# Optimization experiments

Measured on AMD Instinct MI355X. Metric: run time of the kernel, lower is better.

Reference implementation:

```python
import jax, jax.numpy as jnp
import numpy as np

DIM = 512
HEADS = 8
DHEAD = DIM // HEADS
M = DIM // 2          # num_landmarks = 256
ITERS = 6             # pinv iterations
KSIZE = 33            # residual conv kernel (seq axis)
EPS = 1e-5            # LayerNorm eps (torch default)


def moore_penrose_pinv(a, iters=ITERS):
    # a: [b, h, m, m]; iterative Newton-Schulz style pseudo-inverse
    abs_a = jnp.abs(a)
    col = abs_a.sum(-1).max()   # global max of row-sums
    row = abs_a.sum(-2).max()   # global max of col-sums
    z = jnp.swapaxes(a, -1, -2) / (col * row)
    I = jnp.eye(a.shape[-1], dtype=a.dtype)

    def body(z, _):
        az = a @ z
        z = 0.25 * z @ (13.0 * I - az @ (15.0 * I - az @ (7.0 * I - az)))
        return z, None

    z, _ = jax.lax.scan(body, z, None, length=iters)
    return z


def res_conv(v, conv_w):
    # v: [b, h, n, d] treated as NCHW (C=heads), depthwise kernel (33, 1)
    return jax.lax.conv_general_dilated(
        v, conv_w, window_strides=(1, 1),
        padding=((KSIZE // 2, KSIZE // 2), (0, 0)),
        dimension_numbers=('NCHW', 'OIHW', 'NCHW'),
        feature_group_count=HEADS)


def setup_inputs() -> dict:
    key = jax.random.key(0)
    ks = jax.random.split(key, 5)
    b, n = 4, 4096  # n % M == 0 -> no padding branch
    x = jax.random.normal(ks[0], (b, n, DIM), jnp.float32)
    norm_w = jnp.ones((DIM,), jnp.float32)
    norm_b = jnp.zeros((DIM,), jnp.float32)
    Wqkv = jax.random.normal(ks[1], (DIM, 3 * DIM), jnp.float32) * (DIM ** -0.5)
    Wout = jax.random.normal(ks[2], (DIM, DIM), jnp.float32) * (DIM ** -0.5)
    bout = jnp.zeros((DIM,), jnp.float32)
    conv_w = jax.random.normal(ks[3], (HEADS, 1, KSIZE, 1), jnp.float32) * 0.05
    return {"x": x, "norm_w": norm_w, "norm_b": norm_b,
            "Wqkv": Wqkv, "Wout": Wout, "bout": bout, "conv_w": conv_w}


def reference(x, norm_w, norm_b, Wqkv, Wout, bout, conv_w):
    b, n, dim = x.shape
    # LayerNorm
    mu = x.mean(-1, keepdims=True)
    var = ((x - mu) ** 2).mean(-1, keepdims=True)
    xn = (x - mu) * jax.lax.rsqrt(var + EPS) * norm_w + norm_b

    # QKV projection, split heads: [b, h, n, d]
    qkv = xn @ Wqkv
    q, k, v = jnp.split(qkv, 3, axis=-1)
    sh = lambda t: t.reshape(b, n, HEADS, DHEAD).transpose(0, 2, 1, 3)
    q, k, v = sh(q), sh(k), sh(v)
    q = q * (DHEAD ** -0.5)

    # landmarks: mean over consecutive segments of length l = n // M
    l = n // M
    q_l = q.reshape(b, HEADS, M, l, DHEAD).mean(3)  # [b,h,m,d]
    k_l = k.reshape(b, HEADS, M, l, DHEAD).mean(3)

    sim1 = jnp.einsum('bhid,bhjd->bhij', q, k_l)    # [b,h,n,m]
    sim2 = jnp.einsum('bhid,bhjd->bhij', q_l, k_l)  # [b,h,m,m]
    sim3 = jnp.einsum('bhid,bhjd->bhij', q_l, k)    # [b,h,m,n]
    a1 = jax.nn.softmax(sim1, axis=-1)
    a2 = jax.nn.softmax(sim2, axis=-1)
    a3 = jax.nn.softmax(sim3, axis=-1)

    a2_inv = moore_penrose_pinv(a2)
    out = (a1 @ a2_inv) @ (a3 @ v)                  # [b,h,n,d]
    out = out + res_conv(v, conv_w)                  # residual depthwise conv on v

    out = out.transpose(0, 2, 1, 3).reshape(b, n, dim)
    out = out @ Wout + bout                          # to_out (dropout = identity in eval)
    return x + out                                   # TransLayer residual
```

## Files before the change

### kernel.cpp

```cpp
#include <hip/hip_runtime.h>
#include <hip/hip_bf16.h>

#define BB 4
#define NN 4096
#define DIMM 512
#define HH 8
#define DD 64
#define MM 256
#define LL 16
#define BHH 32
#define NROW (BB*NN)
#define KS 33

typedef __attribute__((ext_vector_type(8))) short short8;
typedef __attribute__((ext_vector_type(4))) float float4v;

static __device__ __forceinline__ unsigned short bf16_bits(float v) {
    __hip_bfloat16 h = __float2bfloat16(v);
    return *reinterpret_cast<unsigned short*>(&h);
}

static __device__ __forceinline__ void gl_lds16(const void* g, void* l) {
    __builtin_amdgcn_global_load_lds((const __attribute__((address_space(1))) void*)g,
                                     (__attribute__((address_space(3))) void*)l, 16, 0, 0);
}

static __device__ __forceinline__ void bar_nv() {
    asm volatile("s_waitcnt lgkmcnt(0)\ns_barrier" ::: "memory");
}

static __device__ __forceinline__ int xcd_swz(int hw, int nwg) {
    return (hw & 7) * (nwg >> 3) + (hw >> 3);
}

__launch_bounds__(256)
__global__ void ln_kernel(const float* __restrict__ x,
                          const float* __restrict__ w,
                          const float* __restrict__ bvec,
                          __hip_bfloat16* __restrict__ xn) {
    int row = blockIdx.x;
    int t = threadIdx.x;
    const float* xr = x + (long)row * DIMM;
    float v0 = xr[t];
    float v1 = xr[t + 256];
    __shared__ float red[256];
    red[t] = v0 + v1;
    __syncthreads();
    for (int off = 128; off > 0; off >>= 1) { if (t < off) red[t] += red[t + off]; __syncthreads(); }
    float mu = red[0] * (1.0f / DIMM);
    __syncthreads();
    float d0 = v0 - mu, d1 = v1 - mu;
    red[t] = d0 * d0 + d1 * d1;
    __syncthreads();
    for (int off = 128; off > 0; off >>= 1) { if (t < off) red[t] += red[t + off]; __syncthreads(); }
    float var = red[0] * (1.0f / DIMM);
    float rs = rsqrtf(var + 1e-5f);
    xn[(long)row * DIMM + t]       = __float2bfloat16(d0 * rs * w[t]       + bvec[t]);
    xn[(long)row * DIMM + t + 256] = __float2bfloat16(d1 * rs * w[t + 256] + bvec[t + 256]);
}

__launch_bounds__(256)
__global__ void transpose_bf16(const float* __restrict__ in, __hip_bfloat16* __restrict__ outp,
                               int K, int N) {
    __shared__ float tile[32][33];
    int k0 = blockIdx.y * 32, n0 = blockIdx.x * 32;
    int tx = threadIdx.x & 31, ty = threadIdx.x >> 5;
    #pragma unroll
    for (int i = 0; i < 32; i += 8)
        tile[ty + i][tx] = in[(long)(k0 + ty + i) * N + n0 + tx];
    __syncthreads();
    #pragma unroll
    for (int i = 0; i < 32; i += 8)
        outp[(long)(n0 + ty + i) * K + k0 + tx] = __float2bfloat16(tile[tx][ty + i]);
}

enum { EPI_NONE = 0, EPI_QKV = 1, EPI_OUT = 2 };

template<int EPI>
__launch_bounds__(256)
__global__ void gemm_mfma(const __hip_bfloat16* __restrict__ A,
                          const __hip_bfloat16* __restrict__ Bt,
                          float* __restrict__ C, int M, int N, int K,
                          const float* __restrict__ bias,
                          const float* __restrict__ resid,
                          __hip_bfloat16* __restrict__ qb,
                          __hip_bfloat16* __restrict__ kb,
                          __hip_bfloat16* __restrict__ vtb) {
    __shared__ __hip_bfloat16 As[128][64];
    __shared__ __hip_bfloat16 Bs[128][64];
    const int t = threadIdx.x;
    const int hw = blockIdx.y * gridDim.x + blockIdx.x;
    const int lg = xcd_swz(hw, gridDim.x * gridDim.y);
    const int m0 = (lg / gridDim.x) * 128, n0 = (lg % gridDim.x) * 128;
    const int wave = t >> 6, lane = t & 63;
    const int wrow = wave >> 1, wcol = wave & 1;
    const int lm = lane & 15, quad = lane >> 4;
    const int wbase = wave * 64;

    const __hip_bfloat16* gA[4];
    const __hip_bfloat16* gB[4];
    __hip_bfloat16* lA[4];
    __hip_bfloat16* lB[4];
    #pragma unroll
    for (int p = 0; p < 4; ++p) {
        int idx = t + p * 256;
        int r = idx >> 3;
        int csrc = ((idx & 7) ^ (r & 7)) * 8;
        int cb = (p * 256 + wbase) * 8;
        gA[p] = &A[(long)(m0 + r) * K + csrc];
        gB[p] = &Bt[(long)(n0 + r) * K + csrc];
        lA[p] = &As[0][0] + cb;
        lB[p] = &Bs[0][0] + cb;
    }

    const __hip_bfloat16* pA[2][4];
    const __hip_bfloat16* pB[2][4];
    #pragma unroll
    for (int i = 0; i < 4; ++i) {
        int ra = wrow * 64 + i * 16 + lm;
        int rb = wcol * 64 + i * 16 + lm;
        int ca = quad ^ (ra & 3), ra2 = (ra >> 2) & 1;
        int cb2 = quad ^ (rb & 3), rb2 = (rb >> 2) & 1;
        pA[0][i] = &As[ra][(4 * ra2       + ca)  * 8];
        pA[1][i] = &As[ra][(4 * (1 - ra2) + ca)  * 8];
        pB[0][i] = &Bs[rb][(4 * rb2       + cb2) * 8];
        pB[1][i] = &Bs[rb][(4 * (1 - rb2) + cb2) * 8];
    }

    float4v acc[4][4] = {};

    for (int k0 = 0; k0 < K; k0 += 64) {
        #pragma unroll
        for (int p = 0; p < 4; ++p) {
            gl_lds16(gA[p], lA[p]);
            gl_lds16(gB[p], lB[p]);
            gA[p] += 64;
            gB[p] += 64;
        }
        __syncthreads();
        #pragma unroll
        for (int ksu = 0; ksu < 2; ++ksu) {
            short8 af[4], bfr[4];
            #pragma unroll
            for (int i = 0; i < 4; ++i) {
                af[i]  = *(const short8*)pA[ksu][i];
                bfr[i] = *(const short8*)pB[ksu][i];
            }
            #pragma unroll
            for (int i = 0; i < 4; ++i)
                #pragma unroll
                for (int j = 0; j < 4; ++j)
                    acc[i][j] = __builtin_amdgcn_mfma_f32_16x16x32_bf16(af[i], bfr[j], acc[i][j], 0, 0, 0);
        }
        __syncthreads();
    }

    #pragma unroll
    for (int i = 0; i < 4; ++i) {
        #pragma unroll
        for (int j = 0; j < 4; ++j) {
            int rowb = m0 + wrow * 64 + i * 16 + quad * 4;
            int col  = n0 + wcol * 64 + j * 16 + lm;
            if (EPI == EPI_QKV) {
                int b = rowb >> 12, seq = rowb & (NN - 1);
                int which = col >> 9, rem = col & 511;
                int h = rem >> 6, dd = rem & 63;
                int bh = b * HH + h;
                if (which == 0) {
                    #pragma unroll
                    for (int r = 0; r < 4; ++r)
                        qb[((long)bh * NN + seq + r) * DD + dd] = __float2bfloat16(acc[i][j][r] * 0.125f);
                } else if (which == 1) {
                    #pragma unroll
                    for (int r = 0; r < 4; ++r)
                        kb[((long)bh * NN + seq + r) * DD + dd] = __float2bfloat16(acc[i][j][r]);
                } else {
                    union { unsigned long long u; unsigned short s[4]; } pk;
                    #pragma unroll
                    for (int r = 0; r < 4; ++r) pk.s[r] = bf16_bits(acc[i][j][r]);
                    *(unsigned long long*)&vtb[((long)bh * DD + dd) * NN + seq] = pk.u;
                }
            } else {
                #pragma unroll
                for (int r = 0; r < 4; ++r) {
                    int row = rowb + r;
                    C[(long)row * N + col] = acc[i][j][r] + bias[col] + resid[(long)row * N + col];
                }
            }
        }
    }
}

__launch_bounds__(256)
__global__ void gemm_pinv(const __hip_bfloat16* __restrict__ A,
                          const __hip_bfloat16* __restrict__ Bt,
                          __hip_bfloat16* __restrict__ CnBf,
                          float* __restrict__ CnF,
                          __hip_bfloat16* __restrict__ CTbf,
                          float diag, float sgn, float scale) {
    __shared__ __hip_bfloat16 As[64][256];
    __shared__ __hip_bfloat16 Bs[64][256];
    const int t = threadIdx.x;
    const int hw = (blockIdx.z * 4 + blockIdx.y) * 4 + blockIdx.x;
    const int lg = xcd_swz(hw, 512);
    const long base = (long)(lg >> 4) << 16;
    const int m0 = ((lg >> 2) & 3) * 64, n0 = (lg & 3) * 64;
    const int wave = t >> 6, lane = t & 63;
    const int wr = wave >> 1, wc = wave & 1;
    const int lm = lane & 15, quad = lane >> 4;
    const __hip_bfloat16* Ab = A + base;
    const __hip_bfloat16* Bb = Bt + base;

    #pragma unroll
    for (int p = 0; p < 8; ++p) {
        int idx = t + p * 256;
        int r = idx >> 5;
        int csrc = ((idx & 31) ^ (r & 7)) * 8;
        int cb = idx * 8;
        gl_lds16(&Ab[(long)(m0 + r) * 256 + csrc], &As[0][0] + cb);
        gl_lds16(&Bb[(long)(n0 + r) * 256 + csrc], &Bs[0][0] + cb);
    }

    const char* pA[2][2];
    const char* pB[2][2];
    #pragma unroll
    for (int i = 0; i < 2; ++i) {
        int ra = wr * 32 + i * 16 + lm;
        int rb = wc * 32 + i * 16 + lm;
        int ca = quad ^ (ra & 3), ra2 = (ra >> 2) & 1;
        int cb2 = quad ^ (rb & 3), rb2 = (rb >> 2) & 1;
        pA[0][i] = (const char*)&As[ra][(4 * ra2       + ca)  * 8];
        pA[1][i] = (const char*)&As[ra][(4 * (1 - ra2) + ca)  * 8];
        pB[0][i] = (const char*)&Bs[rb][(4 * rb2       + cb2) * 8];
        pB[1][i] = (const char*)&Bs[rb][(4 * (1 - rb2) + cb2) * 8];
    }
    __syncthreads();

    float4v acc[2][2] = {};
    #pragma unroll
    for (int ksu = 0; ksu < 8; ++ksu) {
        short8 af[2], bfr[2];
        #pragma unroll
        for (int i = 0; i < 2; ++i) {
            af[i]  = *(const short8*)(pA[ksu & 1][i] + (ksu >> 1) * 128);
            bfr[i] = *(const short8*)(pB[ksu & 1][i] + (ksu >> 1) * 128);
        }
        #pragma unroll
        for (int i = 0; i < 2; ++i)
            #pragma unroll
            for (int j = 0; j < 2; ++j)
                acc[i][j] = __builtin_amdgcn_mfma_f32_16x16x32_bf16(af[i], bfr[j], acc[i][j], 0, 0, 0);
    }

    #pragma unroll
    for (int i = 0; i < 2; ++i)
        #pragma unroll
        for (int j = 0; j < 2; ++j) {
            const int rowb = wr * 32 + i * 16 + quad * 4;
            const int col  = wc * 32 + j * 16 + lm;
            union { unsigned long long u; unsigned short s[4]; } pk;
            #pragma unroll
            for (int r = 0; r < 4; ++r) {
                float v = acc[i][j][r] * scale;
                long off = base + (long)(m0 + rowb + r) * 256 + n0 + col;
                if (CnBf) CnBf[off] = __float2bfloat16(v);
                if (CnF)  CnF[off]  = v;
                float tv = sgn * v + ((m0 + rowb + r) == (n0 + col) ? diag : 0.0f);
                pk.s[r] = bf16_bits(tv);
            }
            if (CTbf)
                *(unsigned long long*)&CTbf[base + (long)(n0 + col) * 256 + m0 + rowb] = pk.u;
        }
}

__launch_bounds__(256)
__global__ void pinv_prep(const float* __restrict__ a2, const float* __restrict__ scl,
                          __hip_bfloat16* __restrict__ a2bf, __hip_bfloat16* __restrict__ z0T,
                          __hip_bfloat16* __restrict__ z0n) {
    __shared__ float tl[64][65];
    const int t = threadIdx.x;
    const long base = (long)blockIdx.z << 16;
    const int i0 = blockIdx.y * 64, j0 = blockIdx.x * 64;
    float s = scl[0];
    #pragma unroll
    for (int p = 0; p < 16; ++p) {
        int idx = t + p * 256;
        int r = idx >> 6, c = idx & 63;
        long off = base + (long)(i0 + r) * 256 + j0 + c;
        float v = a2[off];
        a2bf[off] = __float2bfloat16(v);
        float zv = v * s;
        z0T[off] = __float2bfloat16(zv);
        tl[r][c] = zv;
    }
    __syncthreads();
    int r = t & 63;
    #pragma unroll
    for (int u = 0; u < 16; ++u) {
        int c = u * 4 + (t >> 6);
        z0n[base + (long)(j0 + c) * 256 + i0 + r] = __float2bfloat16(tl[r][c]);
    }
}

template<int EPI, bool TRANSB>
__launch_bounds__(256)
__global__ void gemm64(const float* __restrict__ A, const float* __restrict__ Bm,
                       float* __restrict__ C,
                       int M, int N, int K, long sA, long sB, long sC, float alpha) {
    const int gx = gridDim.x, gxy = gridDim.x * gridDim.y;
    const int hw = blockIdx.z * gxy + blockIdx.y * gx + blockIdx.x;
    const int lg = xcd_swz(hw, gxy * gridDim.z);
    const int bz = lg / gxy;
    const int rem = lg % gxy;
    const float* Ab = A + (long)bz * sA;
    const float* Bb = Bm + (long)bz * sB;
    float* Cb = C + (long)bz * sC;

    __shared__ float As[16][64];
    __shared__ float Bs[16][64];

    const int tid = threadIdx.x;
    const int tx = tid & 15;
    const int ty = tid >> 4;
    const int m0 = (rem / gx) * 64;
    const int n0 = (rem % gx) * 64;

    float acc[4][4] = {};

    for (int k0 = 0; k0 < K; k0 += 16) {
        {
            int r  = tid >> 2;
            int kk = (tid & 3) * 4;
            float4 va = *(const float4*)(Ab + (long)(m0 + r) * K + k0 + kk);
            As[kk + 0][r] = va.x; As[kk + 1][r] = va.y; As[kk + 2][r] = va.z; As[kk + 3][r] = va.w;
        }
        if (!TRANSB) {
            int kk = tid >> 4;
            int j  = (tid & 15) * 4;
            float4 vb = *(const float4*)(Bb + (long)(k0 + kk) * N + n0 + j);
            Bs[kk][j + 0] = vb.x; Bs[kk][j + 1] = vb.y; Bs[kk][j + 2] = vb.z; Bs[kk][j + 3] = vb.w;
        } else {
            int j  = tid >> 2;
            int kk = (tid & 3) * 4;
            float4 vb = *(const float4*)(Bb + (long)(n0 + j) * K + k0 + kk);
            Bs[kk + 0][j] = vb.x; Bs[kk + 1][j] = vb.y; Bs[kk + 2][j] = vb.z; Bs[kk + 3][j] = vb.w;
        }
        __syncthreads();
        #pragma unroll
        for (int kk = 0; kk < 16; ++kk) {
            float a0 = As[kk][ty * 4 + 0], a1 = As[kk][ty * 4 + 1];
            float a2 = As[kk][ty * 4 + 2], a3 = As[kk][ty * 4 + 3];
            float b0 = Bs[kk][tx * 4 + 0], b1 = Bs[kk][tx * 4 + 1];
            float b2 = Bs[kk][tx * 4 + 2], b3 = Bs[kk][tx * 4 + 3];
            acc[0][0] += a0 * b0; acc[0][1] += a0 * b1; acc[0][2] += a0 * b2; acc[0][3] += a0 * b3;
            acc[1][0] += a1 * b0; acc[1][1] += a1 * b1; acc[1][2] += a1 * b2; acc[1][3] += a1 * b3;
            acc[2][0] += a2 * b0; acc[2][1] += a2 * b1; acc[2][2] += a2 * b2; acc[2][3] += a2 * b3;
            acc[3][0] += a3 * b0; acc[3][1] += a3 * b1; acc[3][2] += a3 * b2; acc[3][3] += a3 * b3;
        }
        __syncthreads();
    }

    #pragma unroll
    for (int r = 0; r < 4; ++r)
        #pragma unroll
        for (int c = 0; c < 4; ++c)
            Cb[(long)(m0 + ty * 4 + r) * N + n0 + tx * 4 + c] = acc[r][c] * alpha;
}

__global__ void landmark_kernel(const __hip_bfloat16* __restrict__ qb,
                                const __hip_bfloat16* __restrict__ kb,
                                float* __restrict__ q_l, float* __restrict__ k_l,
                                __hip_bfloat16* __restrict__ q_lb,
                                __hip_bfloat16* __restrict__ k_lb) {
    int bh = blockIdx.x >> 8;
    int m  = blockIdx.x & 255;
    int d  = threadIdx.x;
    const __hip_bfloat16* src = (blockIdx.y ? kb : qb) + ((long)bh * NN + m * LL) * DD + d;
    float s = 0.f;
    #pragma unroll
    for (int t = 0; t < LL; ++t) s += __bfloat162float(src[(long)t * DD]);
    s *= (1.0f / LL);
    long off = ((long)bh * MM + m) * DD + d;
    if (blockIdx.y) { k_l[off] = s; k_lb[off] = __float2bfloat16(s); }
    else            { q_l[off] = s; q_lb[off] = __float2bfloat16(s); }
}

__launch_bounds__(256)
__global__ void softmax256_kernel(float* __restrict__ a) {
    long row = blockIdx.x;
    int t = threadIdx.x;
    float* r = a + row * 256;
    float v = r[t];
    __shared__ float red[256];
    red[t] = v;
    __syncthreads();
    for (int off = 128; off > 0; off >>= 1) { if (t < off) red[t] = fmaxf(red[t], red[t + off]); __syncthreads(); }
    float mx = red[0];
    __syncthreads();
    float e = __expf(v - mx);
    red[t] = e;
    __syncthreads();
    for (int off = 128; off > 0; off >>= 1) { if (t < off) red[t] += red[t + off]; __syncthreads(); }
    r[t] = e / red[0];
}

__launch_bounds__(256)
__global__ void redmax_kernel(const float* __restrict__ a2, float* __restrict__ red) {
    int blk = blockIdx.x;
    int bh = blk >> 3, cg = blk & 7;
    int t = threadIdx.x;
    const float* Ab = a2 + ((long)bh << 16) + cg * 32;
    int c = t & 31, rg = t >> 5;
    float s = 0.f;
    for (int r = rg * 32; r < rg * 32 + 32; ++r) s += Ab[(long)r * 256 + c];
    __shared__ float m[256];
    m[t] = s;
    __syncthreads();
    if (t < 32) {
        float cs = 0.f;
        #pragma unroll
        for (int g = 0; g < 8; ++g) cs += m[t + 32 * g];
        m[t] = cs;
    }
    __syncthreads();
    if (t == 0) {
        float mx = m[0];
        #pragma unroll
        for (int i = 1; i < 32; ++i) mx = fmaxf(mx, m[i]);
        red[blk] = mx;
    }
}

__launch_bounds__(256)
__global__ void scale_kernel(const float* __restrict__ red, float* __restrict__ scl) {
    __shared__ float b[256];
    int t = threadIdx.x;
    b[t] = red[t];
    __syncthreads();
    for (int off = 128; off > 0; off >>= 1) {
        if (t < off) b[t] = fmaxf(b[t], b[t + off]);
        __syncthreads();
    }
    if (t == 0) scl[0] = 1.0f / b[0];
}

__launch_bounds__(256)
__global__ void a3v_mfma(const __hip_bfloat16* __restrict__ qlb,
                         const __hip_bfloat16* __restrict__ kb,
                         const __hip_bfloat16* __restrict__ vtb,
                         float* __restrict__ opart, float* __restrict__ lpart) {
    const int hw = blockIdx.y * 16 + blockIdx.x;
    const int lg = xcd_swz(hw, 512);
    const int bh = lg >> 4;
    const int mt = (lg >> 2) & 3;
    const int ns = lg & 3;
    const int t = threadIdx.x;
    const int wave = t >> 6, lane = t & 63;
    const int wr = wave >> 1, wc = wave & 1;
    const int lm = lane & 15, quad = lane >> 4;
    const int r8 = t >> 3, c8 = (t & 7) * 8;

    __shared__ __hip_bfloat16 Qs[64][72];
    __shared__ __hip_bfloat16 Ks[64][72];
    __shared__ __hip_bfloat16 Vt[64][72];
    __shared__ __hip_bfloat16 Ps[64][72];
    __shared__ float lredS[64][2];

    {
        const __hip_bfloat16* qbase = qlb + ((long)bh * MM + mt * 64) * DD;
        *(uint4*)&Qs[r8][c8]      = *(const uint4*)&qbase[(long)r8 * DD + c8];
        *(uint4*)&Qs[r8 + 32][c8] = *(const uint4*)&qbase[(long)(r8 + 32) * DD + c8];
    }

    float4v acc[2][2] = {};
    float lacc[2][4] = {};
    const __hip_bfloat16* kbase = kb + ((long)bh * NN + ns * 1024) * DD;
    const __hip_bfloat16* vbase = vtb + (long)bh * DD * NN + ns * 1024;

    uint4 kv0 = *(const uint4*)&kbase[(long)r8 * DD + c8];
    uint4 kv1 = *(const uint4*)&kbase[(long)(r8 + 32) * DD + c8];
    uint4 vv0 = *(const uint4*)&vbase[(long)r8 * NN + c8];
    uint4 vv1 = *(const uint4*)&vbase[(long)(r8 + 32) * NN + c8];
    bar_nv();

    for (int ch = 0; ch < 16; ++ch) {
        *(uint4*)&Ks[r8][c8]      = kv0;
        *(uint4*)&Ks[r8 + 32][c8] = kv1;
        *(uint4*)&Vt[r8][c8]      = vv0;
        *(uint4*)&Vt[r8 + 32][c8] = vv1;
        if (ch < 15) {
            kv0 = *(const uint4*)&kbase[(long)((ch + 1) * 64 + r8) * DD + c8];
            kv1 = *(const uint4*)&kbase[(long)((ch + 1) * 64 + r8 + 32) * DD + c8];
            vv0 = *(const uint4*)&vbase[(long)r8 * NN + (ch + 1) * 64 + c8];
            vv1 = *(const uint4*)&vbase[(long)(r8 + 32) * NN + (ch + 1) * 64 + c8];
        }
        bar_nv();

        float4v s[2][2] = {};
        #pragma unroll
        for (int ks = 0; ks < 64; ks += 32) {
            short8 af[2], bfr[2];
            #pragma unroll
            for (int i = 0; i < 2; ++i) {
                af[i]  = *(const short8*)&Qs[wr * 32 + i * 16 + lm][ks + quad * 8];
                bfr[i] = *(const short8*)&Ks[wc * 32 + i * 16 + lm][ks + quad * 8];
            }
            #pragma unroll
            for (int i = 0; i < 2; ++i)
                #pragma unroll
                for (int j = 0; j < 2; ++j)
                    s[i][j] = __builtin_amdgcn_mfma_f32_16x16x32_bf16(af[i], bfr[j], s[i][j], 0, 0, 0);
        }
        #pragma unroll
        for (int i = 0; i < 2; ++i)
            #pragma unroll
            for (int j = 0; j < 2; ++j)
                #pragma unroll
                for (int r2 = 0; r2 < 4; ++r2) {
                    float e = __expf(s[i][j][r2]);
                    lacc[i][r2] += e;
                    Ps[wr * 32 + i * 16 + quad * 4 + r2][wc * 32 + j * 16 + lm] = __float2bfloat16(e);
                }
        bar_nv();

        #pragma unroll
        for (int ks = 0; ks < 64; ks += 32) {
            short8 af[2], bfr[2];
            #pragma unroll
            for (int i = 0; i < 2; ++i) {
                af[i]  = *(const short8*)&Ps[wr * 32 + i * 16 + lm][ks + quad * 8];
                bfr[i] = *(const short8*)&Vt[wc * 32 + i * 16 + lm][ks + quad * 8];
            }
            #pragma unroll
            for (int i = 0; i < 2; ++i)
                #pragma unroll
                for (int j = 0; j < 2; ++j)
                    acc[i][j] = __builtin_amdgcn_mfma_f32_16x16x32_bf16(af[i], bfr[j], acc[i][j], 0, 0, 0);
        }
        bar_nv();
    }

    #pragma unroll
    for (int i = 0; i < 2; ++i)
        #pragma unroll
        for (int r2 = 0; r2 < 4; ++r2) {
            float s = lacc[i][r2];
            s += __shfl_xor(s, 1);
            s += __shfl_xor(s, 2);
            s += __shfl_xor(s, 4);
            s += __shfl_xor(s, 8);
            if (lm == 0) lredS[wr * 32 + i * 16 + quad * 4 + r2][wc] = s;
        }
    __syncthreads();
    if (t < 64)
        lpart[((bh * 4 + mt) * 4 + ns) * 64 + t] = lredS[t][0] + lredS[t][1];
    const long pbase = ((long)((bh * 4 + mt) * 4 + ns)) << 12;
    #pragma unroll
    for (int i = 0; i < 2; ++i)
        #pragma unroll
        for (int j = 0; j < 2; ++j)
            #pragma unroll
            for (int r2 = 0; r2 < 4; ++r2)
                opart[pbase + (long)(wr * 32 + i * 16 + quad * 4 + r2) * 64 + wc * 32 + j * 16 + lm] = acc[i][j][r2];
}

__global__ void a3v_combine(const float* __restrict__ opart, const float* __restrict__ lpart,
                            float* __restrict__ a3v) {
    int idx = blockIdx.x * 256 + threadIdx.x;
    int d  = idx & 63;
    int m  = (idx >> 6) & 255;
    int bh = idx >> 14;
    int mt = m >> 6, r = m & 63;
    int pb = (bh * 4 + mt) * 4;
    float osum = 0.f, lsum = 0.f;
    #pragma unroll
    for (int ns = 0; ns < 4; ++ns) {
        osum += opart[(((long)(pb + ns)) << 12) + r * 64 + d];
        lsum += lpart[(pb + ns) * 64 + r];
    }
    a3v[((long)bh * MM + m) * DD + d] = osum / lsum;
}

__launch_bounds__(256)
__global__ void wmT_kernel(const float* __restrict__ wm, __hip_bfloat16* __restrict__ wtb) {
    __shared__ float tile[64][65];
    const int bh = blockIdx.x;
    const int t = threadIdx.x;
    for (int mc = 0; mc < 4; ++mc) {
        #pragma unroll
        for (int p = 0; p < 16; ++p) {
            int idx = t + p * 256;
            int r = idx >> 6, c = idx & 63;
            tile[r][c] = wm[((long)bh * MM + mc * 64 + r) * DD + c];
        }
        __syncthreads();
        #pragma unroll
        for (int p = 0; p < 16; ++p) {
            int idx = t + p * 256;
            int dd = idx >> 6, m = idx & 63;
            wtb[((long)bh * DD + dd) * MM + mc * 64 + m] = __float2bfloat16(tile[m][dd]);
        }
        __syncthreads();
    }
}

__launch_bounds__(256)
__global__ void attn_out_mfma(const __hip_bfloat16* __restrict__ qb,
                              const __hip_bfloat16* __restrict__ klb,
                              const __hip_bfloat16* __restrict__ wtb,
                              const __hip_bfloat16* __restrict__ vtb,
                              const float* __restrict__ convw,
                              __hip_bfloat16* __restrict__ ctx) {
    const int hw = blockIdx.y * 64 + blockIdx.x;
    const int lg = xcd_swz(hw, 2048);
    const int bh = lg >> 6;
    const int b = bh >> 3, h = bh & 7;
    const int i0 = (lg & 63) * 64;
    const int t = threadIdx.x;
    const int wave = t >> 6, lane = t & 63;
    const int wr = wave >> 1, wc = wave & 1;
    const int lm = lane & 15, quad = lane >> 4;
    const int r8 = t >> 3, c8 = (t & 7) * 8;

    __shared__ __hip_bfloat16 Qs[64][72];
    __shared__ __hip_bfloat16 KW[2][64][72];
    __shared__ __hip_bfloat16 Ps[64][72];
    __shared__ __hip_bfloat16 Vc[64][104];
    __shared__ float lredS[64][2];
    __shared__ float dsum[64];
    __shared__ float cwS[KS];
    __hip_bfloat16 (*Tpl)[104] = reinterpret_cast<__hip_bfloat16 (*)[104]>(&KW[0][0][0]);

    if (t < KS) cwS[t] = convw[h * KS + t];

    {
        const __hip_bfloat16* qbase = qb + ((long)bh * NN + i0) * DD;
        *(uint4*)&Qs[r8][c8]      = *(const uint4*)&qbase[(long)r8 * DD + c8];
        *(uint4*)&Qs[r8 + 32][c8] = *(const uint4*)&qbase[(long)(r8 + 32) * DD + c8];
    }
    {
        for (int c = t; c < 768; c += 256) {
            int dd = c / 12, u = c - dd * 12;
            int g0 = i0 - 16 + u * 8;
            const __hip_bfloat16* vrow = vtb + ((long)bh * DD + dd) * NN;
            __align__(16) __hip_bfloat16 tmp[8];
            if (g0 >= 0 && g0 + 8 <= NN) {
                *(uint4*)tmp = *(const uint4*)&vrow[g0];
            } else {
                #pragma unroll
                for (int e = 0; e < 8; ++e) {
                    int g = g0 + e;
                    tmp[e] = (g >= 0 && g < NN) ? vrow[g] : __float2bfloat16(0.f);
                }
            }
            *(uint4*)&Vc[dd][u * 8] = *(uint4*)tmp;
        }
    }
    __syncthreads();

    {
        int r  = t >> 2;
        int c0 = (t & 3) * 24;
        #pragma unroll
        for (int u = 0; u < 12; ++u) {
            int c = c0 + u * 2;
            int d0 = c - r, d1 = c + 1 - r;
            unsigned short lo = (d0 >= 0 && d0 < KS) ? bf16_bits(cwS[d0]) : (unsigned short)0;
            unsigned short hi = (d1 >= 0 && d1 < KS) ? bf16_bits(cwS[d1]) : (unsigned short)0;
            *(unsigned*)&Tpl[r][c] = ((unsigned)hi << 16) | lo;
        }
    }
    bar_nv();

    const __hip_bfloat16* klbase = klb + (long)bh * MM * DD;
    const __hip_bfloat16* wbase  = wtb + (long)bh * DD * MM;
    uint4 kv0 = *(const uint4*)&klbase[(long)r8 * DD + c8];
    uint4 kv1 = *(const uint4*)&klbase[(long)(r8 + 32) * DD + c8];
    uint4 wv0 = *(const uint4*)&wbase[(long)r8 * MM + c8];
    uint4 wv1 = *(const uint4*)&wbase[(long)(r8 + 32) * MM + c8];

    float4v accC[2][2] = {};
    #pragma unroll
    for (int ks = 0; ks < 96; ks += 32) {
        short8 af[2], bfr[2];
        #pragma unroll
        for (int i = 0; i < 2; ++i) {
            af[i]  = *(const short8*)&Tpl[wr * 32 + i * 16 + lm][ks + quad * 8];
            bfr[i] = *(const short8*)&Vc[wc * 32 + i * 16 + lm][ks + quad * 8];
        }
        #pragma unroll
        for (int i = 0; i < 2; ++i)
            #pragma unroll
            for (int j = 0; j < 2; ++j)
                accC[i][j] = __builtin_amdgcn_mfma_f32_16x16x32_bf16(af[i], bfr[j], accC[i][j], 0, 0, 0);
    }
    bar_nv();

    float4v acc[2][2] = {};
    float lacc[2][4] = {};

    for (int ch = 0; ch < 4; ++ch) {
        *(uint4*)&KW[0][r8][c8]      = kv0;
        *(uint4*)&KW[0][r8 + 32][c8] = kv1;
        *(uint4*)&KW[1][r8][c8]      = wv0;
        *(uint4*)&KW[1][r8 + 32][c8] = wv1;
        if (ch < 3) {
            kv0 = *(const uint4*)&klbase[(long)((ch + 1) * 64 + r8) * DD + c8];
            kv1 = *(const uint4*)&klbase[(long)((ch + 1) * 64 + r8 + 32) * DD + c8];
            wv0 = *(const uint4*)&wbase[(long)r8 * MM + (ch + 1) * 64 + c8];
            wv1 = *(const uint4*)&wbase[(long)(r8 + 32) * MM + (ch + 1) * 64 + c8];
        }
        bar_nv();

        float4v s[2][2] = {};
        #pragma unroll
        for (int ks = 0; ks < 64; ks += 32) {
            short8 af[2], bfr[2];
            #pragma unroll
            for (int i = 0; i < 2; ++i) {
                af[i]  = *(const short8*)&Qs[wr * 32 + i * 16 + lm][ks + quad * 8];
                bfr[i] = *(const short8*)&KW[0][wc * 32 + i * 16 + lm][ks + quad * 8];
            }
            #pragma unroll
            for (int i = 0; i < 2; ++i)
                #pragma unroll
                for (int j = 0; j < 2; ++j)
                    s[i][j] = __builtin_amdgcn_mfma_f32_16x16x32_bf16(af[i], bfr[j], s[i][j], 0, 0, 0);
        }
        #pragma unroll
        for (int i = 0; i < 2; ++i)
            #pragma unroll
            for (int j = 0; j < 2; ++j)
                #pragma unroll
                for (int r2 = 0; r2 < 4; ++r2) {
                    float e = __expf(s[i][j][r2]);
                    lacc[i][r2] += e;
                    Ps[wr * 32 + i * 16 + quad * 4 + r2][wc * 32 + j * 16 + lm] = __float2bfloat16(e);
                }
        bar_nv();

        #pragma unroll
        for (int ks = 0; ks < 64; ks += 32) {
            short8 af[2], bfr[2];
            #pragma unroll
            for (int i = 0; i < 2; ++i) {
                af[i]  = *(const short8*)&Ps[wr * 32 + i * 16 + lm][ks + quad * 8];
                bfr[i] = *(const short8*)&KW[1][wc * 32 + i * 16 + lm][ks + quad * 8];
            }
            #pragma unroll
            for (int i = 0; i < 2; ++i)
                #pragma unroll
                for (int j = 0; j < 2; ++j)
                    acc[i][j] = __builtin_amdgcn_mfma_f32_16x16x32_bf16(af[i], bfr[j], acc[i][j], 0, 0, 0);
        }
        bar_nv();
    }

    #pragma unroll
    for (int i = 0; i < 2; ++i)
        #pragma unroll
        for (int r2 = 0; r2 < 4; ++r2) {
            float s = lacc[i][r2];
            s += __shfl_xor(s, 1);
            s += __shfl_xor(s, 2);
            s += __shfl_xor(s, 4);
            s += __shfl_xor(s, 8);
            if (lm == 0) lredS[wr * 32 + i * 16 + quad * 4 + r2][wc] = s;
        }
    __syncthreads();
    if (t < 64) dsum[t] = 1.0f / (lredS[t][0] + lredS[t][1]);
    __syncthreads();

    #pragma unroll
    for (int j = 0; j < 2; ++j) {
        int dd = wc * 32 + j * 16 + lm;
        #pragma unroll
        for (int i = 0; i < 2; ++i) {
            int R = wr * 32 + i * 16 + quad * 4;
            #pragma unroll
            for (int r2 = 0; r2 < 4; ++r2) {
                int row = R + r2;
                ctx[((long)b * NN + i0 + row) * DIMM + h * DD + dd] =
                    __float2bfloat16(acc[i][j][r2] * dsum[row] + accC[i][j][r2]);
            }
        }
    }
}

extern "C" void kernel_launch(void* const* d_in, const int* in_sizes, int n_in,
                              void* d_out, int out_size, void* d_ws, size_t ws_size,
                              hipStream_t stream) {
    const float* x      = (const float*)d_in[0];
    const float* norm_w = (const float*)d_in[1];
    const float* norm_b = (const float*)d_in[2];
    const float* Wqkv   = (const float*)d_in[3];
    const float* Wout   = (const float*)d_in[4];
    const float* bout   = (const float*)d_in[5];
    const float* conv_w = (const float*)d_in[6];
    float* out = (float*)d_out;

    float* ws = (float*)d_ws;
    size_t o = 0;
    auto alloc = [&](size_t n) { float* p = ws + o; o += n; return p; };
    auto allocb = [&](size_t n) { return (__hip_bfloat16*)alloc((n + 1) / 2); };

    __hip_bfloat16* xn_bf  = allocb((size_t)NROW * DIMM);
    __hip_bfloat16* wqt_bf = allocb((size_t)3 * DIMM * DIMM);
    __hip_bfloat16* wot_bf = allocb((size_t)DIMM * DIMM);
    __hip_bfloat16* ctx_bf = allocb((size_t)NROW * DIMM);
    __hip_bfloat16* q_bf   = allocb((size_t)BHH * NN * DD);
    __hip_bfloat16* k_bf   = allocb((size_t)BHH * NN * DD);
    __hip_bfloat16* vt_bf  = allocb((size_t)BHH * DD * NN);
    __hip_bfloat16* qlb    = allocb((size_t)BHH * MM * DD);
    __hip_bfloat16* klb    = allocb((size_t)BHH * MM * DD);
    __hip_bfloat16* wt_bf  = allocb((size_t)BHH * DD * MM);
    float* q_l  = alloc((size_t)BHH * MM * DD);
    float* k_l  = alloc((size_t)BHH * MM * DD);
    float* a2   = alloc((size_t)BHH * MM * MM);
    float* zb   = alloc((size_t)BHH * MM * MM);
    float* az   = alloc((size_t)BHH * MM * MM);
    float* gb   = alloc((size_t)BHH * MM * MM);
    float* tb   = alloc((size_t)BHH * MM * MM);
    float* z2   = alloc((size_t)BHH * MM * MM);
    float* a3v  = alloc((size_t)BHH * MM * DD);
    float* wm   = alloc((size_t)BHH * MM * DD);
    float* opart = alloc((size_t)BHH * 4 * 4 * 64 * 64);
    float* lpart = alloc((size_t)BHH * 4 * 4 * 64);
    float* red  = alloc(256);
    float* scl  = alloc(64);

    const size_t HB = 1048576;
    __hip_bfloat16* a2bf = (__hip_bfloat16*)az;
    __hip_bfloat16* znA  = (__hip_bfloat16*)(az + HB);
    __hip_bfloat16* znB  = (__hip_bfloat16*)gb;
    __hip_bfloat16* zTA  = (__hip_bfloat16*)(gb + HB);
    __hip_bfloat16* zTB  = (__hip_bfloat16*)tb;
    __hip_bfloat16* azbf = (__hip_bfloat16*)(tb + HB);
    __hip_bfloat16* g1T  = (__hip_bfloat16*)z2;
    __hip_bfloat16* g2T  = (__hip_bfloat16*)(z2 + HB);
    __hip_bfloat16* g3T  = (__hip_bfloat16*)opart;

    ln_kernel<<<NROW, 256, 0, stream>>>(x, norm_w, norm_b, xn_bf);

    transpose_bf16<<<dim3(3 * DIMM / 32, DIMM / 32), 256, 0, stream>>>(Wqkv, wqt_bf, DIMM, 3 * DIMM);
    transpose_bf16<<<dim3(DIMM / 32, DIMM / 32), 256, 0, stream>>>(Wout, wot_bf, DIMM, DIMM);

    gemm_mfma<EPI_QKV><<<dim3(3 * DIMM / 128, NROW / 128), 256, 0, stream>>>(
        xn_bf, wqt_bf, nullptr, NROW, 3 * DIMM, DIMM,
        nullptr, nullptr, q_bf, k_bf, vt_bf);

    landmark_kernel<<<dim3(BHH * MM, 2), 64, 0, stream>>>(q_bf, k_bf, q_l, k_l, qlb, klb);

    gemm64<EPI_NONE, true><<<dim3(4, 4, BHH), 256, 0, stream>>>(
        q_l, k_l, a2, MM, MM, DD, (long)MM * DD, (long)MM * DD, (long)MM * MM, 1.0f);

    softmax256_kernel<<<BHH * MM, 256, 0, stream>>>(a2);

    redmax_kernel<<<BHH * 8, 256, 0, stream>>>(a2, red);
    scale_kernel<<<1, 256, 0, stream>>>(red, scl);

    dim3 g512(4, 4, BHH);
    pinv_prep<<<g512, 256, 0, stream>>>(a2, scl, a2bf, zTA, znA);

    __hip_bfloat16 *zn = znA, *zT = zTA, *zn2 = znB, *zT2 = zTB;
    for (int it = 0; it < 6; ++it) {
        gemm_pinv<<<g512, 256, 0, stream>>>(a2bf, zT, azbf, nullptr, g1T, 7.0f, -1.0f, 1.0f);
        gemm_pinv<<<g512, 256, 0, stream>>>(azbf, g1T, nullptr, nullptr, g2T, 15.0f, -1.0f, 1.0f);
        gemm_pinv<<<g512, 256, 0, stream>>>(azbf, g2T, nullptr, nullptr, g3T, 13.0f, -1.0f, 1.0f);
        gemm_pinv<<<g512, 256, 0, stream>>>(zn, g3T, zn2, (it == 5) ? zb : nullptr, zT2,
                                            0.0f, 1.0f, 0.25f);
        __hip_bfloat16* tmp;
        tmp = zn; zn = zn2; zn2 = tmp;
        tmp = zT; zT = zT2; zT2 = tmp;
    }

    a3v_mfma<<<dim3(16, BHH), 256, 0, stream>>>(qlb, k_bf, vt_bf, opart, lpart);
    a3v_combine<<<BHH * MM * DD / 256, 256, 0, stream>>>(opart, lpart, a3v);

    gemm64<EPI_NONE, false><<<dim3(1, 4, BHH), 256, 0, stream>>>(
        zb, a3v, wm, MM, DD, MM, (long)MM * MM, (long)MM * DD, (long)MM * DD, 1.0f);
    wmT_kernel<<<BHH, 256, 0, stream>>>(wm, wt_bf);

    attn_out_mfma<<<dim3(NN / 64, BHH), 256, 0, stream>>>(
        q_bf, klb, wt_bf, vt_bf, conv_w, ctx_bf);

    gemm_mfma<EPI_OUT><<<dim3(DIMM / 128, NROW / 128), 256, 0, stream>>>(
        ctx_bf, wot_bf, out, NROW, DIMM, DIMM,
        bout, x, nullptr, nullptr, nullptr);
}
```

Measured before the change: 403.4 us.

## Double-buffer LDS tiles in MFMA GEMM to overlap global loads with compute

The GEMM kernel now keeps two LDS buffers for the A and B tiles. It issues the next k-tile's global-to-LDS loads before computing on the current tile, and uses a partial vmcnt wait plus raw barriers in place of full __syncthreads. The aim is to hide global load latency behind the MFMA work. In exchange, LDS use doubles to 64KB per block, which may lower occupancy, and correctness depends on the hand-written waitcnt and barrier ordering.

Measured after the change: 405.5 us. No clear change (+0.5%).

```diff
diff --git a/kernel.cpp b/kernel.cpp
--- a/kernel.cpp
+++ b/kernel.cpp
@@ -86,8 +86,8 @@
                           __hip_bfloat16* __restrict__ qb,
                           __hip_bfloat16* __restrict__ kb,
                           __hip_bfloat16* __restrict__ vtb) {
-    __shared__ __hip_bfloat16 As[128][64];
-    __shared__ __hip_bfloat16 Bs[128][64];
+    __shared__ __hip_bfloat16 As[2][128][64];
+    __shared__ __hip_bfloat16 Bs[2][128][64];
     const int t = threadIdx.x;
     const int hw = blockIdx.y * gridDim.x + blockIdx.x;
     const int lg = xcd_swz(hw, gridDim.x * gridDim.y);
@@ -109,42 +109,60 @@
         int cb = (p * 256 + wbase) * 8;
         gA[p] = &A[(long)(m0 + r) * K + csrc];
         gB[p] = &Bt[(long)(n0 + r) * K + csrc];
-        lA[p] = &As[0][0] + cb;
-        lB[p] = &Bs[0][0] + cb;
-    }
-
-    const __hip_bfloat16* pA[2][4];
-    const __hip_bfloat16* pB[2][4];
+        lA[p] = &As[0][0][0] + cb;
+        lB[p] = &Bs[0][0][0] + cb;
+    }
+
+    const char* pA[2][4];
+    const char* pB[2][4];
     #pragma unroll
     for (int i = 0; i < 4; ++i) {
         int ra = wrow * 64 + i * 16 + lm;
         int rb = wcol * 64 + i * 16 + lm;
         int ca = quad ^ (ra & 3), ra2 = (ra >> 2) & 1;
         int cb2 = quad ^ (rb & 3), rb2 = (rb >> 2) & 1;
-        pA[0][i] = &As[ra][(4 * ra2       + ca)  * 8];
-        pA[1][i] = &As[ra][(4 * (1 - ra2) + ca)  * 8];
-        pB[0][i] = &Bs[rb][(4 * rb2       + cb2) * 8];
-        pB[1][i] = &Bs[rb][(4 * (1 - rb2) + cb2) * 8];
+        pA[0][i] = (const char*)&As[0][ra][(4 * ra2       + ca)  * 8];
+        pA[1][i] = (const char*)&As[0][ra][(4 * (1 - ra2) + ca)  * 8];
+        pB[0][i] = (const char*)&Bs[0][rb][(4 * rb2       + cb2) * 8];
+        pB[1][i] = (const char*)&Bs[0][rb][(4 * (1 - rb2) + cb2) * 8];
     }
 
     float4v acc[4][4] = {};
-
-    for (int k0 = 0; k0 < K; k0 += 64) {
-        #pragma unroll
-        for (int p = 0; p < 4; ++p) {
-            gl_lds16(gA[p], lA[p]);
-            gl_lds16(gB[p], lB[p]);
-            gA[p] += 64;
-            gB[p] += 64;
-        }
-        __syncthreads();
+    const int kiters = K >> 6;
+
+    #pragma unroll
+    for (int p = 0; p < 4; ++p) {
+        gl_lds16(gA[p], lA[p]);
+        gl_lds16(gB[p], lB[p]);
+        gA[p] += 64;
+        gB[p] += 64;
+    }
+
+    for (int k = 0; k < kiters; ++k) {
+        const int cur = k & 1;
+        if (k + 1 < kiters) {
+            const int nxt = cur ^ 1;
+            #pragma unroll
+            for (int p = 0; p < 4; ++p) {
+                gl_lds16(gA[p], lA[p] + nxt * 8192);
+                gl_lds16(gB[p], lB[p] + nxt * 8192);
+                gA[p] += 64;
+                gB[p] += 64;
+            }
+            asm volatile("s_waitcnt vmcnt(8)" ::: "memory");
+        } else {
+            asm volatile("s_waitcnt vmcnt(0)" ::: "memory");
+        }
+        __builtin_amdgcn_s_barrier();
+
+        const int bo = cur * 16384;
         #pragma unroll
         for (int ksu = 0; ksu < 2; ++ksu) {
             short8 af[4], bfr[4];
             #pragma unroll
             for (int i = 0; i < 4; ++i) {
-                af[i]  = *(const short8*)pA[ksu][i];
-                bfr[i] = *(const short8*)pB[ksu][i];
+                af[i]  = *(const short8*)(pA[ksu][i] + bo);
+                bfr[i] = *(const short8*)(pB[ksu][i] + bo);
             }
             #pragma unroll
             for (int i = 0; i < 4; ++i)
@@ -152,7 +170,7 @@
                 for (int j = 0; j < 4; ++j)
                     acc[i][j] = __builtin_amdgcn_mfma_f32_16x16x32_bf16(af[i], bfr[j], acc[i][j], 0, 0, 0);
         }
-        __syncthreads();
+        bar_nv();
     }
 
     #pragma unroll
```

## Restructure pinv iteration to compute next A·Z alongside Z update

Applied to the files above, without the earlier changes.

The Newton-Schulz iteration is rewritten so that each step's final GEMM computes both Z' = 0.25·Z·T3 and P' = A·Z' = 0.25·P·T3 in one merged launch. This uses the identity that A·Z·T3 equals P·T3, so the separate A·Z GEMM at the start of each iteration drops out. Per iteration that means three launches instead of four, with one extra GEMM done once before the loop. Computing P by recurrence in bf16 rather than directly from A may let rounding error accumulate across iterations.

After: 390.4 us. 1.03x faster.

```diff
diff --git a/kernel.cpp b/kernel.cpp
--- a/kernel.cpp
+++ b/kernel.cpp
@@ -274,6 +274,96 @@
 }
 
 __launch_bounds__(256)
+__global__ void gemm_pinv2(const __hip_bfloat16* __restrict__ zA,
+                           const __hip_bfloat16* __restrict__ pAg,
+                           const __hip_bfloat16* __restrict__ t3T,
+                           __hip_bfloat16* __restrict__ zOut,
+                           float* __restrict__ zF,
+                           __hip_bfloat16* __restrict__ pOut,
+                           __hip_bfloat16* __restrict__ t1T) {
+    __shared__ __hip_bfloat16 As[64][256];
+    __shared__ __hip_bfloat16 Bs[64][256];
+    const int t = threadIdx.x;
+    const int hw = blockIdx.y * 16 + blockIdx.x;
+    const int lg = xcd_swz(hw, 1024);
+    const int pair = lg >> 5;
+    const int half = (lg >> 4) & 1;
+    const int tile = lg & 15;
+    const long base = (long)pair << 16;
+    const int m0 = (tile >> 2) * 64, n0 = (tile & 3) * 64;
+    const int wave = t >> 6, lane = t & 63;
+    const int wr = wave >> 1, wc = wave & 1;
+    const int lm = lane & 15, quad = lane >> 4;
+    const __hip_bfloat16* Ab = (half ? pAg : zA) + base;
+    const __hip_bfloat16* Bb = t3T + base;
+
+    #pragma unroll
+    for (int p = 0; p < 8; ++p) {
+        int idx = t + p * 256;
+        int r = idx >> 5;
+        int csrc = ((idx & 31) ^ (r & 7)) * 8;
+        int cb = idx * 8;
+        gl_lds16(&Ab[(long)(m0 + r) * 256 + csrc], &As[0][0] + cb);
+        gl_lds16(&Bb[(long)(n0 + r) * 256 + csrc], &Bs[0][0] + cb);
+    }
+
+    const char* pA[2][2];
+    const char* pB[2][2];
+    #pragma unroll
+    for (int i = 0; i < 2; ++i) {
+        int ra = wr * 32 + i * 16 + lm;
+        int rb = wc * 32 + i * 16 + lm;
+        int ca = quad ^ (ra & 3), ra2 = (ra >> 2) & 1;
+        int cb2 = quad ^ (rb & 3), rb2 = (rb >> 2) & 1;
+        pA[0][i] = (const char*)&As[ra][(4 * ra2       + ca)  * 8];
+        pA[1][i] = (const char*)&As[ra][(4 * (1 - ra2) + ca)  * 8];
+        pB[0][i] = (const char*)&Bs[rb][(4 * rb2       + cb2) * 8];
+        pB[1][i] = (const char*)&Bs[rb][(4 * (1 - rb2) + cb2) * 8];
+    }
+    __syncthreads();
+
+    float4v acc[2][2] = {};
+    #pragma unroll
+    for (int ksu = 0; ksu < 8; ++ksu) {
+        short8 af[2], bfr[2];
+        #pragma unroll
+        for (int i = 0; i < 2; ++i) {
+            af[i]  = *(const short8*)(pA[ksu & 1][i] + (ksu >> 1) * 128);
+            bfr[i] = *(const short8*)(pB[ksu & 1][i] + (ksu >> 1) * 128);
+        }
+        #pragma unroll
+        for (int i = 0; i < 2; ++i)
+            #pragma unroll
+            for (int j = 0; j < 2; ++j)
+                acc[i][j] = __builtin_amdgcn_mfma_f32_16x16x32_bf16(af[i], bfr[j], acc[i][j], 0, 0, 0);
+    }
+
+    #pragma unroll
+    for (int i = 0; i < 2; ++i)
+        #pragma unroll
+        for (int j = 0; j < 2; ++j) {
+            const int rowb = wr * 32 + i * 16 + quad * 4;
+            const int col  = wc * 32 + j * 16 + lm;
+            union { unsigned long long u; unsigned short s[4]; } pk;
+            #pragma unroll
+            for (int r = 0; r < 4; ++r) {
+                float v = acc[i][j][r] * 0.25f;
+                long off = base + (long)(m0 + rowb + r) * 256 + n0 + col;
+                if (half == 0) {
+                    zOut[off] = __float2bfloat16(v);
+                    if (zF) zF[off] = v;
+                } else {
+                    pOut[off] = __float2bfloat16(v);
+                    float tv = -v + ((m0 + rowb + r) == (n0 + col) ? 7.0f : 0.0f);
+                    pk.s[r] = bf16_bits(tv);
+                }
+            }
+            if (half)
+                *(unsigned long long*)&t1T[base + (long)(n0 + col) * 256 + m0 + rowb] = pk.u;
+        }
+}
+
+__launch_bounds__(256)
 __global__ void pinv_prep(const float* __restrict__ a2, const float* __restrict__ scl,
                           __hip_bfloat16* __restrict__ a2bf, __hip_bfloat16* __restrict__ z0T,
                           __hip_bfloat16* __restrict__ z0n) {
@@ -831,14 +921,13 @@
 
     const size_t HB = 1048576;
     __hip_bfloat16* a2bf = (__hip_bfloat16*)az;
-    __hip_bfloat16* znA  = (__hip_bfloat16*)(az + HB);
-    __hip_bfloat16* znB  = (__hip_bfloat16*)gb;
-    __hip_bfloat16* zTA  = (__hip_bfloat16*)(gb + HB);
-    __hip_bfloat16* zTB  = (__hip_bfloat16*)tb;
-    __hip_bfloat16* azbf = (__hip_bfloat16*)(tb + HB);
-    __hip_bfloat16* g1T  = (__hip_bfloat16*)z2;
-    __hip_bfloat16* g2T  = (__hip_bfloat16*)(z2 + HB);
-    __hip_bfloat16* g3T  = (__hip_bfloat16*)opart;
+    __hip_bfloat16* z0Tb = (__hip_bfloat16*)(az + HB);
+    __hip_bfloat16* zpA  = (__hip_bfloat16*)gb;
+    __hip_bfloat16* zpB  = (__hip_bfloat16*)(gb + HB);
+    __hip_bfloat16* PnA  = (__hip_bfloat16*)tb;
+    __hip_bfloat16* t1A  = (__hip_bfloat16*)(tb + HB);
+    __hip_bfloat16* t2T  = (__hip_bfloat16*)z2;
+    __hip_bfloat16* t3Tb = (__hip_bfloat16*)(z2 + HB);
 
     ln_kernel<<<NROW, 256, 0, stream>>>(x, norm_w, norm_b, xn_bf);
 
@@ -860,18 +949,21 @@
     scale_kernel<<<1, 256, 0, stream>>>(red, scl);
 
     dim3 g512(4, 4, BHH);
-    pinv_prep<<<g512, 256, 0, stream>>>(a2, scl, a2bf, zTA, znA);
-
-    __hip_bfloat16 *zn = znA, *zT = zTA, *zn2 = znB, *zT2 = zTB;
+    pinv_prep<<<g512, 256, 0, stream>>>(a2, scl, a2bf, z0Tb, zpA);
+
+    gemm_pinv<<<g512, 256, 0, stream>>>(a2bf, z0Tb, PnA, nullptr, t1A, 7.0f, -1.0f, 1.0f);
+    __hip_bfloat16 *zi = zpA, *zo = zpB;
+    __hip_bfloat16 *Pc = PnA, *Pn2 = a2bf;
+    __hip_bfloat16 *t1c = t1A, *t1n = z0Tb;
     for (int it = 0; it < 6; ++it) {
-        gemm_pinv<<<g512, 256, 0, stream>>>(a2bf, zT, azbf, nullptr, g1T, 7.0f, -1.0f, 1.0f);
-        gemm_pinv<<<g512, 256, 0, stream>>>(azbf, g1T, nullptr, nullptr, g2T, 15.0f, -1.0f, 1.0f);
-        gemm_pinv<<<g512, 256, 0, stream>>>(azbf, g2T, nullptr, nullptr, g3T, 13.0f, -1.0f, 1.0f);
-        gemm_pinv<<<g512, 256, 0, stream>>>(zn, g3T, zn2, (it == 5) ? zb : nullptr, zT2,
-                                            0.0f, 1.0f, 0.25f);
+        gemm_pinv<<<g512, 256, 0, stream>>>(Pc, t1c, nullptr, nullptr, t2T, 15.0f, -1.0f, 1.0f);
+        gemm_pinv<<<g512, 256, 0, stream>>>(Pc, t2T, nullptr, nullptr, t3Tb, 13.0f, -1.0f, 1.0f);
+        gemm_pinv2<<<dim3(16, 64), 256, 0, stream>>>(zi, Pc, t3Tb, zo,
+                                                     (it == 5) ? zb : nullptr, Pn2, t1n);
         __hip_bfloat16* tmp;
-        tmp = zn; zn = zn2; zn2 = tmp;
-        tmp = zT; zT = zT2; zT2 = tmp;
+        tmp = zi; zi = zo; zo = tmp;
+        tmp = Pc; Pc = Pn2; Pn2 = tmp;
+        tmp = t1c; t1c = t1n; t1n = tmp;
     }
 
     a3v_mfma<<<dim3(16, BHH), 256, 0, stream>>>(qlb, k_bf, vt_bf, opart, lpart);
```
